# Kernel optimization log

Measured on AMD Instinct MI355X. Metric: run time of the kernel, lower is better.

The kernel has to match this reference:

```python
import jax, jax.numpy as jnp
import numpy as np

D_MODEL = 1024
N_HEADS = 16
D_K = D_MODEL // N_HEADS
D_FF = 4096
B, S = 4, 2048


def setup_inputs() -> dict:
    key = jax.random.key(0)
    ks = jax.random.split(key, 16)
    s = 0.02
    inp = {
        "x": jax.random.normal(ks[0], (B, S, D_MODEL), dtype=jnp.float32),
        "wq": jax.random.normal(ks[1], (D_MODEL, D_MODEL), dtype=jnp.float32) * s,
        "bq": jnp.zeros((D_MODEL,), jnp.float32),
        "wk": jax.random.normal(ks[2], (D_MODEL, D_MODEL), dtype=jnp.float32) * s,
        "bk": jnp.zeros((D_MODEL,), jnp.float32),
        "wv": jax.random.normal(ks[3], (D_MODEL, D_MODEL), dtype=jnp.float32) * s,
        "bv": jnp.zeros((D_MODEL,), jnp.float32),
        "wo": jax.random.normal(ks[4], (D_MODEL, D_MODEL), dtype=jnp.float32) * s,
        "bo": jnp.zeros((D_MODEL,), jnp.float32),
        "w1": jax.random.normal(ks[5], (D_MODEL, D_FF), dtype=jnp.float32) * s,
        "b1": jnp.zeros((D_FF,), jnp.float32),
        "w2": jax.random.normal(ks[6], (D_FF, D_MODEL), dtype=jnp.float32) * s,
        "b2": jnp.zeros((D_MODEL,), jnp.float32),
        "ln1_g": jnp.ones((D_MODEL,), jnp.float32),
        "ln1_b": jnp.zeros((D_MODEL,), jnp.float32),
        "ln2_g": jnp.ones((D_MODEL,), jnp.float32),
        "ln2_b": jnp.zeros((D_MODEL,), jnp.float32),
    }
    return inp


def _layernorm(x, g, b, eps=1e-5):
    mu = jnp.mean(x, axis=-1, keepdims=True)
    var = jnp.mean(jnp.square(x - mu), axis=-1, keepdims=True)
    return (x - mu) * jax.lax.rsqrt(var + eps) * g + b


def _attention(h, wq, bq, wk, bk, wv, bv, wo, bo):
    b, s, _ = h.shape
    q = (h @ wq + bq).reshape(b, s, N_HEADS, D_K).transpose(0, 2, 1, 3)
    k = (h @ wk + bk).reshape(b, s, N_HEADS, D_K).transpose(0, 2, 1, 3)
    v = (h @ wv + bv).reshape(b, s, N_HEADS, D_K).transpose(0, 2, 1, 3)
    scores = jnp.einsum('bhqd,bhkd->bhqk', q, k) / jnp.sqrt(jnp.float32(D_K))
    causal = jnp.triu(jnp.ones((s, s), dtype=bool), k=1)  # True above diag
    scores = jnp.where(causal[None, None], -jnp.inf, scores)
    attn = jax.nn.softmax(scores, axis=-1)
    out = jnp.einsum('bhqk,bhkd->bhqd', attn, v)
    out = out.transpose(0, 2, 1, 3).reshape(b, s, D_MODEL)
    return out @ wo + bo


def reference(x, wq, bq, wk, bk, wv, bv, wo, bo, w1, b1, w2, b2,
              ln1_g, ln1_b, ln2_g, ln2_b):
    attn_out = _attention(_layernorm(x, ln1_g, ln1_b), wq, bq, wk, bk, wv, bv, wo, bo)
    x = x + attn_out
    h = _layernorm(x, ln2_g, ln2_b)
    ff = jax.nn.gelu(h @ w1 + b1, approximate=False) @ w2 + b2
    return x + ff
```

## Files before the change

kernel.cpp:

```cpp
#include <hip/hip_runtime.h>
#include <hip/hip_bf16.h>

#define DM   1024
#define DFF  4096
#define NB   4
#define SS   2048
#define NH   16
#define DK   64
#define MROWS (NB*SS)

typedef __attribute__((ext_vector_type(8))) short bfx8;
typedef __attribute__((ext_vector_type(4))) float fx4;
typedef unsigned int u32;
typedef unsigned short u16;

static __device__ __forceinline__ u16 f2bf(float f) {
  union { __hip_bfloat16 h; u16 u; } cv;
  cv.h = __float2bfloat16(f);
  return cv.u;
}
static __device__ __forceinline__ u32 pk2bf(float a, float b) {
  return (u32)f2bf(a) | ((u32)f2bf(b) << 16);
}

static __device__ __forceinline__ void async16(void* lds, const void* g) {
  typedef const __attribute__((address_space(1))) unsigned int* gp_t;
  typedef __attribute__((address_space(3))) unsigned int* lp_t;
  __builtin_amdgcn_global_load_lds((gp_t)g, (lp_t)lds, 16, 0, 0);
}

__global__ __launch_bounds__(256) void k_transpose(const float* __restrict__ in,
                                                   u16* __restrict__ out,
                                                   int K, int N) {
  __shared__ float t[32][33];
  const int n0 = blockIdx.x * 32, k0 = blockIdx.y * 32;
  const int tx = threadIdx.x & 31, ty = threadIdx.x >> 5;
#pragma unroll
  for (int j = 0; j < 4; j++)
    t[ty + j * 8][tx] = in[(size_t)(k0 + ty + j * 8) * N + n0 + tx];
  __syncthreads();
#pragma unroll
  for (int j = 0; j < 4; j++)
    out[(size_t)(n0 + ty + j * 8) * K + k0 + tx] = f2bf(t[tx][ty + j * 8]);
}

__global__ __launch_bounds__(256) void k_layernorm(const float* __restrict__ x,
                                                   const float* __restrict__ g,
                                                   const float* __restrict__ b,
                                                   u16* __restrict__ out) {
  const int row  = blockIdx.x * 4 + (threadIdx.x >> 6);
  const int lane = threadIdx.x & 63;
  const float* xr = x + (size_t)row * DM;
  float4 vb[4];
  float s = 0.f, s2 = 0.f;
#pragma unroll
  for (int j = 0; j < 4; j++) {
    float4 v = *(const float4*)(xr + j * 256 + lane * 4);
    vb[j] = v;
    s  += v.x + v.y + v.z + v.w;
    s2 += v.x * v.x + v.y * v.y + v.z * v.z + v.w * v.w;
  }
#pragma unroll
  for (int off = 1; off < 64; off <<= 1) {
    s  += __shfl_xor(s,  off);
    s2 += __shfl_xor(s2, off);
  }
  const float mu   = s * (1.f / DM);
  const float var  = s2 * (1.f / DM) - mu * mu;
  const float rstd = rsqrtf(var + 1e-5f);
  u16* orow = out + (size_t)row * DM;
#pragma unroll
  for (int j = 0; j < 4; j++) {
    const int col = j * 256 + lane * 4;
    uint2 o;
    o.x = pk2bf((vb[j].x - mu) * rstd * g[col + 0] + b[col + 0],
                (vb[j].y - mu) * rstd * g[col + 1] + b[col + 1]);
    o.y = pk2bf((vb[j].z - mu) * rstd * g[col + 2] + b[col + 2],
                (vb[j].w - mu) * rstd * g[col + 3] + b[col + 3]);
    *(uint2*)(orow + col) = o;
  }
}

template <int EPI, int NWR>
__global__ __launch_bounds__(512, 2) void k_gemm_bt(const u16* __restrict__ A,
                                                    const u16* __restrict__ BT,
                                                    const float* __restrict__ bias0,
                                                    const float* __restrict__ bias1,
                                                    const float* __restrict__ bias2,
                                                    const float* __restrict__ res,
                                                    void* __restrict__ outp,
                                                    int M, int N, int K) {
  constexpr int NWC    = 8 / NWR;
  constexpr int BN     = NWC * 64;
  constexpr int MFRAG  = 256 / NWR / 16;
  constexpr int ABYTES = 256 * 32 * 2;
  constexpr int BBYTES = BN * 32 * 2;
  constexpr int LA     = ABYTES / (512 * 16);
  constexpr int LB     = BBYTES / (512 * 16);
  constexpr int L      = LA + LB;

  __shared__ char Al[4 * ABYTES];
  __shared__ char Bl[4 * BBYTES];

  const int tid = threadIdx.x, wave = tid >> 6, lane = tid & 63;
  const int nwg = gridDim.x * gridDim.y;
  const int bid = blockIdx.y * gridDim.x + blockIdx.x;
  const int swz = (bid & 7) * (nwg >> 3) + (bid >> 3);
  const int m0 = (swz / gridDim.x) * 256, n0 = (swz % gridDim.x) * BN;
  const int wr = wave / NWC, wc = wave % NWC;
  const int wm = wr * (256 / NWR), wn = wc * 64;
  const int la = lane & 15, lg = lane >> 4;
  const int psw = (la >> 1) & 3;

  fx4 acc[MFRAG][4];
#pragma unroll
  for (int i = 0; i < MFRAG; i++)
#pragma unroll
    for (int j = 0; j < 4; j++) acc[i][j] = fx4{0.f, 0.f, 0.f, 0.f};

  const int arow = tid >> 2;
  const int aslot = ((tid & 3) ^ ((tid >> 3) & 3)) * 8;
  const u16* gA = A  + (size_t)(m0 + arow) * K + aslot;
  const u16* gB = BT + (size_t)(n0 + arow) * K + aslot;

  auto stageg = [&](int buf, int kt) {
#pragma unroll
    for (int j = 0; j < LA; j++)
      async16(Al + buf * ABYTES + j * 8192 + wave * 1024, gA + (size_t)(j * 128) * K + kt);
#pragma unroll
    for (int j = 0; j < LB; j++)
      async16(Bl + buf * BBYTES + j * 8192 + wave * 1024, gB + (size_t)(j * 128) * K + kt);
  };

  const int nk = K >> 5;
  stageg(0, 0);
  stageg(1, 32);
  stageg(2, 64);

  for (int t = 0; t < nk; ++t) {
    const int rem = nk - 1 - t;
    if (rem >= 2)      { asm volatile("s_waitcnt vmcnt(%0)" :: "n"(2 * L) : "memory"); }
    else if (rem == 1) { asm volatile("s_waitcnt vmcnt(%0)" :: "n"(L)     : "memory"); }
    else               { asm volatile("s_waitcnt vmcnt(0)" ::: "memory"); }
    __builtin_amdgcn_s_barrier();
    asm volatile("" ::: "memory");

    const char* Ab = (const char*)Al + (t & 3) * ABYTES;
    const char* Bb = (const char*)Bl + (t & 3) * BBYTES;
    bfx8 av[MFRAG], bv[4];
#pragma unroll
    for (int mt = 0; mt < MFRAG; mt++)
      av[mt] = *(const bfx8*)(Ab + (wm + mt * 16 + la) * 64 + (lg ^ psw) * 16);
#pragma unroll
    for (int nt = 0; nt < 4; nt++)
      bv[nt] = *(const bfx8*)(Bb + (wn + nt * 16 + la) * 64 + (lg ^ psw) * 16);

    if (t + 3 < nk) stageg((t + 3) & 3, (t + 3) * 32);

    __builtin_amdgcn_s_setprio(1);
#pragma unroll
    for (int mt = 0; mt < MFRAG; mt++)
#pragma unroll
      for (int nt = 0; nt < 4; nt++)
        acc[mt][nt] = __builtin_amdgcn_mfma_f32_16x16x32_bf16(av[mt], bv[nt], acc[mt][nt], 0, 0, 0);
    __builtin_amdgcn_s_setprio(0);
    asm volatile("" ::: "memory");
  }

  if constexpr (EPI == 4) {
    const int reg = n0 >> 10;
    const float* bp = (reg == 0) ? bias0 : (reg == 1) ? bias1 : bias2;
#pragma unroll
    for (int nt = 0; nt < 4; nt++) {
      const int n  = n0 + wn + nt * 16 + la;
      const int nl = n & 1023;
      const float bs = bp[nl];
      if (reg < 2) {
        u16* base = (u16*)outp + (size_t)reg * (8u * 1024 * 1024);
#pragma unroll
        for (int mt = 0; mt < MFRAG; mt++)
#pragma unroll
          for (int vv = 0; vv < 4; vv++) {
            const int m = m0 + wm + mt * 16 + lg * 4 + vv;
            base[(size_t)m * 1024 + nl] = f2bf(acc[mt][nt][vv] + bs);
          }
      } else {
        const int hh = nl >> 6, d = nl & 63;
#pragma unroll
        for (int mt = 0; mt < MFRAG; mt++) {
          const int m = m0 + wm + mt * 16 + lg * 4;
          const int bb = m >> 11, s = m & 2047;
          u16* vp = (u16*)outp + 16u * 1024 * 1024 +
                    (((size_t)bb * NH + hh) * DK + d) * SS + s;
          uint2 o;
          o.x = pk2bf(acc[mt][nt][0] + bs, acc[mt][nt][1] + bs);
          o.y = pk2bf(acc[mt][nt][2] + bs, acc[mt][nt][3] + bs);
          *(uint2*)vp = o;
        }
      }
    }
  } else {
#pragma unroll
    for (int nt = 0; nt < 4; nt++) {
      const int n = n0 + wn + nt * 16 + la;
      const float bs = bias0[n];
#pragma unroll
      for (int mt = 0; mt < MFRAG; mt++) {
#pragma unroll
        for (int vv = 0; vv < 4; vv++) {
          const int m = m0 + wm + mt * 16 + lg * 4 + vv;
          const float val = acc[mt][nt][vv] + bs;
          const size_t idx = (size_t)m * N + n;
          if constexpr (EPI == 1) {
            ((float*)outp)[idx] = res[idx] + val;
          } else {
            const float gl = 0.5f * val * (1.f + erff(val * 0.70710678118f));
            ((u16*)outp)[idx] = f2bf(gl);
          }
        }
      }
    }
  }
}

__global__ __launch_bounds__(512, 4) void k_attn(const u16* __restrict__ q,
                                                 const u16* __restrict__ k,
                                                 const u16* __restrict__ vt,
                                                 u16* __restrict__ att) {
  __shared__ char sm[65536];
  const int bid = blockIdx.x;
  const int bq = 15 - (bid >> 6);
  const int bh = bid & 63;
  const int b = bh >> 4, h = bh & 15;

  const int tid = threadIdx.x, wave = tid >> 6, lane = tid & 63;
  const int g = wave >> 2, wv4 = wave & 3;
  const int la = lane & 15, lg = lane >> 4;
  const int q0 = bq * 128;

  bfx8 qf[2][2];
#pragma unroll
  for (int qt = 0; qt < 2; qt++) {
    const u16* qp = q + (size_t)(b * SS + q0 + wv4 * 32 + qt * 16 + la) * DM + h * DK + lg * 8;
#pragma unroll
    for (int f = 0; f < 2; f++) qf[qt][f] = *(const bfx8*)(qp + f * 32);
  }

  fx4 acc[2][4];
#pragma unroll
  for (int qt = 0; qt < 2; qt++)
#pragma unroll
    for (int dt = 0; dt < 4; dt++) acc[qt][dt] = fx4{0.f, 0.f, 0.f, 0.f};
  float mold[2] = {-10000.f, -10000.f};
  float lsum[2] = {0.f, 0.f};

  const int srow = lane >> 3;
  const int sslot = (lane & 7) ^ srow;
  const u16* kg0 = k  + (size_t)(b * SS + wv4 * 16 + srow) * DM + h * DK + sslot * 8;
  const u16* vg0 = vt + (size_t)((b * NH + h) * DK + wv4 * 16 + srow) * SS + sslot * 8;
  char* kbase = sm + g * 32768 + wv4 * 2048;
  char* vbase = sm + g * 32768 + 16384 + wv4 * 2048;

  const float c1 = 0.18033688f;
  const int niter = bq + 1;

  auto stage = [&](int buf, int i) {
    const int c0 = (2 * i + g) * 64;
#pragma unroll
    for (int j = 0; j < 2; j++)
      async16(kbase + buf * 8192 + j * 1024, kg0 + (size_t)(c0 + j * 8) * DM);
#pragma unroll
    for (int j = 0; j < 2; j++)
      async16(vbase + buf * 8192 + j * 1024, vg0 + (size_t)(j * 8) * SS + c0);
  };

  stage(0, 0);
  int cur = 0;
  const int sw = la & 7;

  for (int i = 0; i < niter; i++) {
    __syncthreads();
    if (i + 1 < niter) stage(cur ^ 1, i + 1);
    const int c0 = (2 * i + g) * 64;
    const bool msk = (i == niter - 1);
    const char* Kb = sm + g * 32768 + cur * 8192;
    const char* Vb = sm + g * 32768 + 16384 + cur * 8192;

    fx4 st[2][4];
    __builtin_amdgcn_s_setprio(1);
#pragma unroll
    for (int t = 0; t < 4; t++) {
      const char* kr = Kb + (size_t)(t * 16 + la) * 128;
      bfx8 kf0 = *(const bfx8*)(kr + ((0 + lg) ^ sw) * 16);
      bfx8 kf1 = *(const bfx8*)(kr + ((4 + lg) ^ sw) * 16);
#pragma unroll
      for (int qt = 0; qt < 2; qt++) {
        fx4 z = fx4{0.f, 0.f, 0.f, 0.f};
        z = __builtin_amdgcn_mfma_f32_16x16x32_bf16(kf0, qf[qt][0], z, 0, 0, 0);
        z = __builtin_amdgcn_mfma_f32_16x16x32_bf16(kf1, qf[qt][1], z, 0, 0, 0);
        st[qt][t] = z;
      }
    }
    __builtin_amdgcn_s_setprio(0);

    if (msk) {
#pragma unroll
      for (int qt = 0; qt < 2; qt++) {
        const int qir = q0 + wv4 * 32 + qt * 16 + la;
#pragma unroll
        for (int t = 0; t < 4; t++)
#pragma unroll
          for (int r = 0; r < 4; r++)
            if (c0 + t * 16 + lg * 4 + r > qir) st[qt][t][r] = -1e9f;
      }
    }

    float lmx[2];
#pragma unroll
    for (int qt = 0; qt < 2; qt++) {
      float mx = fmaxf(fmaxf(st[qt][0][0], st[qt][0][1]), fmaxf(st[qt][0][2], st[qt][0][3]));
#pragma unroll
      for (int t = 1; t < 4; t++)
        mx = fmaxf(mx, fmaxf(fmaxf(st[qt][t][0], st[qt][t][1]), fmaxf(st[qt][t][2], st[qt][t][3])));
      lmx[qt] = mx * c1;
    }
    const bool def = (lmx[0] <= mold[0] + 8.f) && (lmx[1] <= mold[1] + 8.f);
    if (!__all(def)) {
#pragma unroll
      for (int qt = 0; qt < 2; qt++) {
        float mx = lmx[qt];
        mx = fmaxf(mx, __shfl_xor(mx, 16));
        mx = fmaxf(mx, __shfl_xor(mx, 32));
        const float mnew  = fmaxf(mold[qt], mx);
        const float scale = exp2f(mold[qt] - mnew);
        mold[qt] = mnew;
        lsum[qt] *= scale;
#pragma unroll
        for (int dt = 0; dt < 4; dt++) {
          acc[qt][dt][0] *= scale; acc[qt][dt][1] *= scale;
          acc[qt][dt][2] *= scale; acc[qt][dt][3] *= scale;
        }
      }
    }
    u32 W[2][4][2];
#pragma unroll
    for (int qt = 0; qt < 2; qt++) {
      float ps = 0.f;
#pragma unroll
      for (int t = 0; t < 4; t++) {
        float p0 = exp2f(fmaf(st[qt][t][0], c1, -mold[qt]));
        float p1 = exp2f(fmaf(st[qt][t][1], c1, -mold[qt]));
        float p2 = exp2f(fmaf(st[qt][t][2], c1, -mold[qt]));
        float p3 = exp2f(fmaf(st[qt][t][3], c1, -mold[qt]));
        ps += (p0 + p1) + (p2 + p3);
        W[qt][t][0] = pk2bf(p0, p1);
        W[qt][t][1] = pk2bf(p2, p3);
      }
      lsum[qt] += ps;
    }

    const int sLo = la + ((lg & 1) << 5);
    const int sHi = sLo + 16;
    const bool tHi = (lg >> 1) & 1;
#pragma unroll
    for (int f = 0; f < 2; f++) {
      bfx8 pf[2];
#pragma unroll
      for (int qt = 0; qt < 2; qt++) {
        const u32 a0 = __shfl(W[qt][2 * f][0], sLo), b0 = __shfl(W[qt][2 * f + 1][0], sLo);
        const u32 a1 = __shfl(W[qt][2 * f][1], sLo), b1 = __shfl(W[qt][2 * f + 1][1], sLo);
        const u32 a2 = __shfl(W[qt][2 * f][0], sHi), b2 = __shfl(W[qt][2 * f + 1][0], sHi);
        const u32 a3 = __shfl(W[qt][2 * f][1], sHi), b3 = __shfl(W[qt][2 * f + 1][1], sHi);
        union { u32 u[4]; bfx8 v; } pu;
        pu.u[0] = tHi ? b0 : a0;
        pu.u[1] = tHi ? b1 : a1;
        pu.u[2] = tHi ? b2 : a2;
        pu.u[3] = tHi ? b3 : a3;
        pf[qt] = pu.v;
      }
      __builtin_amdgcn_s_setprio(1);
#pragma unroll
      for (int dt = 0; dt < 4; dt++) {
        const int row = dt * 16 + la;
        bfx8 vf = *(const bfx8*)(Vb + (size_t)row * 128 + (((f << 2) + lg) ^ sw) * 16);
        acc[0][dt] = __builtin_amdgcn_mfma_f32_16x16x32_bf16(vf, pf[0], acc[0][dt], 0, 0, 0);
        acc[1][dt] = __builtin_amdgcn_mfma_f32_16x16x32_bf16(vf, pf[1], acc[1][dt], 0, 0, 0);
      }
      __builtin_amdgcn_s_setprio(0);
    }
    cur ^= 1;
  }

#pragma unroll
  for (int qt = 0; qt < 2; qt++) {
    lsum[qt] += __shfl_xor(lsum[qt], 16);
    lsum[qt] += __shfl_xor(lsum[qt], 32);
  }

  __syncthreads();
  const int gi = wv4 * 64 + lane;
  float* scr = (float*)sm + (size_t)gi * 36;
  if (g == 1) {
#pragma unroll
    for (int qt = 0; qt < 2; qt++)
#pragma unroll
      for (int dt = 0; dt < 4; dt++)
#pragma unroll
        for (int j = 0; j < 4; j++) scr[qt * 16 + dt * 4 + j] = acc[qt][dt][j];
    scr[32] = mold[0]; scr[33] = mold[1];
    scr[34] = lsum[0]; scr[35] = lsum[1];
  }
  __syncthreads();
  if (g == 0) {
#pragma unroll
    for (int qt = 0; qt < 2; qt++) {
      const float mB = scr[32 + qt], lB = scr[34 + qt];
      const float mN = fmaxf(mold[qt], mB);
      const float sA = exp2f(mold[qt] - mN);
      const float sB = exp2f(mB - mN);
      const float inv = 1.f / (lsum[qt] * sA + lB * sB);
      u16* ob = att + (size_t)(b * SS + q0 + wv4 * 32 + qt * 16 + la) * DM + h * DK + lg * 4;
#pragma unroll
      for (int dt = 0; dt < 4; dt++) {
        float o0 = (acc[qt][dt][0] * sA + scr[qt * 16 + dt * 4 + 0] * sB) * inv;
        float o1 = (acc[qt][dt][1] * sA + scr[qt * 16 + dt * 4 + 1] * sB) * inv;
        float o2 = (acc[qt][dt][2] * sA + scr[qt * 16 + dt * 4 + 2] * sB) * inv;
        float o3 = (acc[qt][dt][3] * sA + scr[qt * 16 + dt * 4 + 3] * sB) * inv;
        uint2 o;
        o.x = pk2bf(o0, o1);
        o.y = pk2bf(o2, o3);
        *(uint2*)(ob + dt * 16) = o;
      }
    }
  }
}

extern "C" void kernel_launch(void* const* d_in, const int* in_sizes, int n_in,
                              void* d_out, int out_size, void* d_ws, size_t ws_size,
                              hipStream_t stream) {
  const float* x    = (const float*)d_in[0];
  const float* wq   = (const float*)d_in[1];
  const float* bq   = (const float*)d_in[2];
  const float* wk   = (const float*)d_in[3];
  const float* bk   = (const float*)d_in[4];
  const float* wv   = (const float*)d_in[5];
  const float* bv   = (const float*)d_in[6];
  const float* wo   = (const float*)d_in[7];
  const float* bo   = (const float*)d_in[8];
  const float* w1   = (const float*)d_in[9];
  const float* b1   = (const float*)d_in[10];
  const float* w2   = (const float*)d_in[11];
  const float* b2   = (const float*)d_in[12];
  const float* ln1g = (const float*)d_in[13];
  const float* ln1b = (const float*)d_in[14];
  const float* ln2g = (const float*)d_in[15];
  const float* ln2b = (const float*)d_in[16];
  float* out = (float*)d_out;

  char* w = (char*)d_ws;
  const size_t MB = 1024ull * 1024ull;
  u16*   wqkv = (u16*)(w + 0 * MB);
  u16*   wot  = (u16*)(w + 6 * MB);
  u16*   w1t  = (u16*)(w + 8 * MB);
  u16*   w2t  = (u16*)(w + 16 * MB);
  float* x2   = (float*)(w + 24 * MB);
  u16*   hb   = (u16*)(w + 56 * MB);
  u16*   qb   = (u16*)(w + 72 * MB);
  u16*   kb   = (u16*)(w + 88 * MB);
  u16*   vtb  = (u16*)(w + 104 * MB);
  u16*   atb  = (u16*)(w + 120 * MB);
  u16*   ffb  = (u16*)(w + 72 * MB);

  k_transpose<<<dim3(32, 32),  256, 0, stream>>>(wq, wqkv,               1024, 1024);
  k_transpose<<<dim3(32, 32),  256, 0, stream>>>(wk, wqkv + 1024 * 1024, 1024, 1024);
  k_transpose<<<dim3(32, 32),  256, 0, stream>>>(wv, wqkv + 2048 * 1024, 1024, 1024);
  k_transpose<<<dim3(32, 32),  256, 0, stream>>>(wo, wot, 1024, 1024);
  k_transpose<<<dim3(128, 32), 256, 0, stream>>>(w1, w1t, 1024, 4096);
  k_transpose<<<dim3(32, 128), 256, 0, stream>>>(w2, w2t, 4096, 1024);

  k_layernorm<<<MROWS / 4, 256, 0, stream>>>(x, ln1g, ln1b, hb);

  k_gemm_bt<4, 4><<<dim3(24, 32), 512, 0, stream>>>(hb, wqkv, bq, bk, bv, nullptr, qb,
                                                    MROWS, 3 * DM, DM);

  k_attn<<<dim3(1024), 512, 0, stream>>>(qb, kb, vtb, atb);

  k_gemm_bt<1, 4><<<dim3(8, 32), 512, 0, stream>>>(atb, wot, bo, nullptr, nullptr, x, x2,
                                                   MROWS, DM, DM);

  k_layernorm<<<MROWS / 4, 256, 0, stream>>>(x2, ln2g, ln2b, hb);

  k_gemm_bt<2, 2><<<dim3(16, 32), 512, 0, stream>>>(hb, w1t, b1, nullptr, nullptr, nullptr, ffb,
                                                    MROWS, DFF, DM);

  k_gemm_bt<1, 4><<<dim3(8, 32), 512, 0, stream>>>(ffb, w2t, b2, nullptr, nullptr, x2, out,
                                                   MROWS, DM, DFF);
}
```

Before: 401.2 us.

## Split GEMM main loop into interleaved load/MFMA phases with staggered A/B prefetch

Restructures the bf16 GEMM K-loop so the wait and barrier move to the end of each iteration. For the NWR==2 variant, each iteration is split into two half-MFMA phases, with the A and B prefetches issued separately between them. The aim is to interleave global loads, LDS reads and MFMA work across waves, so memory latency is hidden behind compute. In exchange, each iteration gains extra barriers, which could add sync overhead.

```diff
diff --git a/kernel.cpp b/kernel.cpp
--- a/kernel.cpp
+++ b/kernel.cpp
@@ -90,17 +90,17 @@
                                                     const float* __restrict__ res,
                                                     void* __restrict__ outp,
                                                     int M, int N, int K) {
-  constexpr int NWC    = 8 / NWR;
-  constexpr int BN     = NWC * 64;
-  constexpr int MFRAG  = 256 / NWR / 16;
-  constexpr int ABYTES = 256 * 32 * 2;
-  constexpr int BBYTES = BN * 32 * 2;
-  constexpr int LA     = ABYTES / (512 * 16);
-  constexpr int LB     = BBYTES / (512 * 16);
-  constexpr int L      = LA + LB;
-
-  __shared__ char Al[4 * ABYTES];
-  __shared__ char Bl[4 * BBYTES];
+  constexpr int NWC   = 8 / NWR;
+  constexpr int BN    = NWC * 64;
+  constexpr int MFRAG = 256 / NWR / 16;
+  constexpr int ABUF  = 256 * 32 * 2;
+  constexpr int BBUF  = BN * 32 * 2;
+  constexpr int SA    = 2;
+  constexpr int SB    = BBUF / 8192;
+  constexpr int S     = SA + SB;
+
+  __shared__ char Al[4 * ABUF];
+  __shared__ char Bl[4 * BBUF];
 
   const int tid = threadIdx.x, wave = tid >> 6, lane = tid & 63;
   const int nwg = gridDim.x * gridDim.y;
@@ -123,48 +123,102 @@
   const u16* gA = A  + (size_t)(m0 + arow) * K + aslot;
   const u16* gB = BT + (size_t)(n0 + arow) * K + aslot;
 
-  auto stageg = [&](int buf, int kt) {
-#pragma unroll
-    for (int j = 0; j < LA; j++)
-      async16(Al + buf * ABYTES + j * 8192 + wave * 1024, gA + (size_t)(j * 128) * K + kt);
-#pragma unroll
-    for (int j = 0; j < LB; j++)
-      async16(Bl + buf * BBYTES + j * 8192 + wave * 1024, gB + (size_t)(j * 128) * K + kt);
+  auto stageA = [&](int buf, int kt) {
+#pragma unroll
+    for (int j = 0; j < SA; j++)
+      async16(Al + buf * ABUF + j * 8192 + wave * 1024, gA + (size_t)(j * 128) * K + kt);
   };
+  auto stageB = [&](int buf, int kt) {
+#pragma unroll
+    for (int j = 0; j < SB; j++)
+      async16(Bl + buf * BBUF + j * 8192 + wave * 1024, gB + (size_t)(j * 128) * K + kt);
+  };
 
   const int nk = K >> 5;
-  stageg(0, 0);
-  stageg(1, 32);
-  stageg(2, 64);
+  stageA(0, 0);  stageB(0, 0);
+  stageA(1, 32); stageB(1, 32);
+  stageA(2, 64); stageB(2, 64);
+  asm volatile("s_waitcnt vmcnt(%0)" :: "n"(2 * S) : "memory");
+  __builtin_amdgcn_s_barrier();
+  asm volatile("" ::: "memory");
 
   for (int t = 0; t < nk; ++t) {
+    const char* Ab = (const char*)Al + (t & 3) * ABUF;
+    const char* Bb = (const char*)Bl + (t & 3) * BBUF;
     const int rem = nk - 1 - t;
-    if (rem >= 2)      { asm volatile("s_waitcnt vmcnt(%0)" :: "n"(2 * L) : "memory"); }
-    else if (rem == 1) { asm volatile("s_waitcnt vmcnt(%0)" :: "n"(L)     : "memory"); }
-    else               { asm volatile("s_waitcnt vmcnt(0)" ::: "memory"); }
-    __builtin_amdgcn_s_barrier();
-    asm volatile("" ::: "memory");
-
-    const char* Ab = (const char*)Al + (t & 3) * ABYTES;
-    const char* Bb = (const char*)Bl + (t & 3) * BBYTES;
-    bfx8 av[MFRAG], bv[4];
-#pragma unroll
-    for (int mt = 0; mt < MFRAG; mt++)
-      av[mt] = *(const bfx8*)(Ab + (wm + mt * 16 + la) * 64 + (lg ^ psw) * 16);
-#pragma unroll
-    for (int nt = 0; nt < 4; nt++)
-      bv[nt] = *(const bfx8*)(Bb + (wn + nt * 16 + la) * 64 + (lg ^ psw) * 16);
-
-    if (t + 3 < nk) stageg((t + 3) & 3, (t + 3) * 32);
-
-    __builtin_amdgcn_s_setprio(1);
-#pragma unroll
-    for (int mt = 0; mt < MFRAG; mt++)
-#pragma unroll
-      for (int nt = 0; nt < 4; nt++)
-        acc[mt][nt] = __builtin_amdgcn_mfma_f32_16x16x32_bf16(av[mt], bv[nt], acc[mt][nt], 0, 0, 0);
-    __builtin_amdgcn_s_setprio(0);
-    asm volatile("" ::: "memory");
+    const bool pf = (t + 3 < nk);
+    const int pb = (t + 3) & 3;
+    const int pk = (t + 3) << 5;
+
+    if constexpr (NWR == 2) {
+      bfx8 av0[4], bv[4];
+#pragma unroll
+      for (int i = 0; i < 4; i++)
+        av0[i] = *(const bfx8*)(Ab + (wm + i * 16 + la) * 64 + (lg ^ psw) * 16);
+#pragma unroll
+      for (int i = 0; i < 4; i++)
+        bv[i] = *(const bfx8*)(Bb + (wn + i * 16 + la) * 64 + (lg ^ psw) * 16);
+      if (pf) stageA(pb, pk);
+      asm volatile("" ::: "memory");
+      __builtin_amdgcn_s_barrier();
+      asm volatile("" ::: "memory");
+      __builtin_amdgcn_s_setprio(1);
+#pragma unroll
+      for (int mt = 0; mt < 4; mt++)
+#pragma unroll
+        for (int nt = 0; nt < 4; nt++)
+          acc[mt][nt] = __builtin_amdgcn_mfma_f32_16x16x32_bf16(av0[mt], bv[nt], acc[mt][nt], 0, 0, 0);
+      __builtin_amdgcn_s_setprio(0);
+      asm volatile("" ::: "memory");
+      __builtin_amdgcn_s_barrier();
+      asm volatile("" ::: "memory");
+      bfx8 av1[4];
+#pragma unroll
+      for (int i = 0; i < 4; i++)
+        av1[i] = *(const bfx8*)(Ab + (wm + (4 + i) * 16 + la) * 64 + (lg ^ psw) * 16);
+      if (pf) stageB(pb, pk);
+      asm volatile("" ::: "memory");
+      __builtin_amdgcn_s_barrier();
+      asm volatile("" ::: "memory");
+      __builtin_amdgcn_s_setprio(1);
+#pragma unroll
+      for (int mt = 0; mt < 4; mt++)
+#pragma unroll
+        for (int nt = 0; nt < 4; nt++)
+          acc[4 + mt][nt] = __builtin_amdgcn_mfma_f32_16x16x32_bf16(av1[mt], bv[nt], acc[4 + mt][nt], 0, 0, 0);
+      __builtin_amdgcn_s_setprio(0);
+      if (rem >= 3)      { asm volatile("s_waitcnt vmcnt(%0)" :: "n"(2 * S) : "memory"); }
+      else if (rem == 2) { asm volatile("s_waitcnt vmcnt(%0)" :: "n"(S)     : "memory"); }
+      else if (rem == 1) { asm volatile("s_waitcnt vmcnt(0)" ::: "memory"); }
+      asm volatile("" ::: "memory");
+      __builtin_amdgcn_s_barrier();
+      asm volatile("" ::: "memory");
+    } else {
+      bfx8 av[4], bv[4];
+#pragma unroll
+      for (int i = 0; i < 4; i++)
+        av[i] = *(const bfx8*)(Ab + (wm + i * 16 + la) * 64 + (lg ^ psw) * 16);
+#pragma unroll
+      for (int i = 0; i < 4; i++)
+        bv[i] = *(const bfx8*)(Bb + (wn + i * 16 + la) * 64 + (lg ^ psw) * 16);
+      if (pf) { stageA(pb, pk); stageB(pb, pk); }
+      asm volatile("" ::: "memory");
+      __builtin_amdgcn_s_barrier();
+      asm volatile("" ::: "memory");
+      __builtin_amdgcn_s_setprio(1);
+#pragma unroll
+      for (int mt = 0; mt < 4; mt++)
+#pragma unroll
+        for (int nt = 0; nt < 4; nt++)
+          acc[mt][nt] = __builtin_amdgcn_mfma_f32_16x16x32_bf16(av[mt], bv[nt], acc[mt][nt], 0, 0, 0);
+      __builtin_amdgcn_s_setprio(0);
+      if (rem >= 3)      { asm volatile("s_waitcnt vmcnt(%0)" :: "n"(2 * S) : "memory"); }
+      else if (rem == 2) { asm volatile("s_waitcnt vmcnt(%0)" :: "n"(S)     : "memory"); }
+      else if (rem == 1) { asm volatile("s_waitcnt vmcnt(0)" ::: "memory"); }
+      asm volatile("" ::: "memory");
+      __builtin_amdgcn_s_barrier();
+      asm volatile("" ::: "memory");
+    }
   }
 
   if constexpr (EPI == 4) {
```

New measurement: 402.2 us. No clear change (+0.2%).
